# Optimization experiments

Hardware: AMD Instinct MI355X
Metric: run time of the kernel (lower is better)

Reference implementation:

```python
import jax, jax.numpy as jnp
import numpy as np

EMB = 1024
H = 16
DH = 64


def setup_inputs() -> dict:
    key = jax.random.key(0)
    ks = jax.random.split(key, 9)
    s = 1.0 / np.sqrt(EMB)
    so = 1.0 / np.sqrt(H * DH)
    return {
        "x": jax.random.normal(ks[0], (4, 2048, EMB), dtype=jnp.float32),
        "Wq": jax.random.uniform(ks[1], (H * DH, EMB), jnp.float32, -s, s),
        "bq": jax.random.uniform(ks[2], (H * DH,), jnp.float32, -s, s),
        "Wk": jax.random.uniform(ks[3], (H * DH, EMB), jnp.float32, -s, s),
        "bk": jax.random.uniform(ks[4], (H * DH,), jnp.float32, -s, s),
        "Wv": jax.random.uniform(ks[5], (H * DH, EMB), jnp.float32, -s, s),
        "bv": jax.random.uniform(ks[6], (H * DH,), jnp.float32, -s, s),
        "Wo": jax.random.uniform(ks[7], (EMB, H * DH), jnp.float32, -so, so),
        "bo": jax.random.uniform(ks[8], (EMB,), jnp.float32, -so, so),
    }


def reference(x, Wq, bq, Wk, bk, Wv, bv, Wo, bo):
    B, S, E = x.shape
    # project and split heads: [B, H, S, Dh]
    def proj(W, b):
        return (jnp.einsum('bse,de->bsd', x, W) + b).reshape(B, S, H, DH).transpose(0, 2, 1, 3)
    q = proj(Wq, bq)
    k = proj(Wk, bk)
    v = proj(Wv, bv)
    scores = jnp.einsum('bhsd,bhtd->bhst', q / jnp.sqrt(jnp.float32(DH)), k)
    attn = jax.nn.softmax(scores, axis=-1)
    out = jnp.einsum('bhst,bhtd->bhsd', attn, v)  # [B,H,S,Dh]
    out = out.transpose(0, 2, 1, 3).reshape(B, S, H * DH)
    return jnp.einsum('bsd,ed->bse', out, Wo) + bo
```

## Files before the change

kernel.cpp:

```cpp
#include <hip/hip_runtime.h>
#include <hip/hip_bf16.h>
#include <stdint.h>

typedef __bf16 bf16x8 __attribute__((ext_vector_type(8)));
typedef float f32x4 __attribute__((ext_vector_type(4)));
typedef float f32x16 __attribute__((ext_vector_type(16)));
typedef uint32_t u32x4 __attribute__((ext_vector_type(4)));

__device__ __forceinline__ ushort f2bf(float f) {
  uint32_t u = __builtin_bit_cast(uint32_t, f);
  u += 0x7FFFu + ((u >> 16) & 1u);
  return (ushort)(u >> 16);
}

__device__ __forceinline__ uint32_t cvtpk(float lo, float hi) {
  uint32_t r;
  asm("v_cvt_pk_bf16_f32 %0, %1, %2" : "=v"(r) : "v"(lo), "v"(hi));
  return r;
}

__device__ __forceinline__ void p32swap(uint32_t& x, uint32_t& y) {
  asm("v_permlane32_swap_b32 %0, %1" : "+v"(x), "+v"(y));
}

__device__ __forceinline__ void gload16(const void* g, void* l) {
  auto gp = reinterpret_cast<const __attribute__((address_space(1))) char*>(
      reinterpret_cast<uintptr_t>(g));
  auto lp = reinterpret_cast<__attribute__((address_space(3))) char*>(
      reinterpret_cast<uintptr_t>(l));
  __builtin_amdgcn_global_load_lds(gp, lp, 16, 0, 0);
}

__device__ __forceinline__ f32x4 mfma16(bf16x8 a, bf16x8 b, f32x4 c) {
  return __builtin_amdgcn_mfma_f32_16x16x32_bf16(a, b, c, 0, 0, 0);
}
__device__ __forceinline__ f32x16 mfma32(bf16x8 a, bf16x8 b, f32x16 c) {
  return __builtin_amdgcn_mfma_f32_32x32x16_bf16(a, b, c, 0, 0, 0);
}

#define VMW(n) do { asm volatile("s_waitcnt vmcnt(" #n ")" ::: "memory"); \
                    __builtin_amdgcn_sched_barrier(0); } while (0)
#define SBAR __builtin_amdgcn_s_barrier()
#define SCHED0 __builtin_amdgcn_sched_barrier(0)

__global__ void cast_all(const float* __restrict__ x,  const float* __restrict__ wq,
                         const float* __restrict__ wk, const float* __restrict__ wv,
                         const float* __restrict__ wo,
                         ushort* __restrict__ xb, ushort* __restrict__ wqkv,
                         ushort* __restrict__ wob) {
  int bid = blockIdx.x;
  const float* src; ushort* dst; int base;
  if (bid < 8192)       { src = x;  dst = xb;              base = bid; }
  else if (bid < 9216)  { src = wq; dst = wqkv;            base = bid - 8192; }
  else if (bid < 10240) { src = wk; dst = wqkv + 1048576;  base = bid - 9216; }
  else if (bid < 11264) { src = wv; dst = wqkv + 2097152;  base = bid - 10240; }
  else                  { src = wo; dst = wob;             base = bid - 11264; }
  int i = (base * 256 + threadIdx.x) * 4;
  float4 v = *(const float4*)(src + i);
  ushort4 o;
  o.x = f2bf(v.x); o.y = f2bf(v.y); o.z = f2bf(v.z); o.w = f2bf(v.w);
  *(ushort4*)(dst + i) = o;
}

template <int MODE>
__global__ __launch_bounds__(512, 2) void gemm_k(
    const ushort* __restrict__ A, const ushort* __restrict__ Bm,
    const float* __restrict__ b0, const float* __restrict__ b1,
    ushort* __restrict__ qo, ushort* __restrict__ ko, ushort* __restrict__ vo,
    float* __restrict__ fo)
{
  __shared__ ushort As[3][128 * 64];
  __shared__ ushort Bs[3][256 * 64];
  const int tid = threadIdx.x;
  const int lane = tid & 63, wid = tid >> 6;
  const int wr = wid >> 2, wc = wid & 3;
  const int l15 = lane & 15, l4 = lane >> 4;

  const int wg = blockIdx.x, nwg = gridDim.x, qch = nwg >> 3;
  const int lid = (wg & 7) * qch + (wg >> 3);
  const int bx = (MODE == 2) ? (lid >> 4) : (lid >> 6);
  const int by = (MODE == 2) ? (lid & 15) : (lid & 63);
  const int m0 = by * 128, n0 = bx * 256;

  const char* Ag = (const char*)(A + (size_t)m0 * 1024);
  const char* Wg = (const char*)(Bm + (size_t)n0 * 1024);

  f32x4 acc[4][4] = {};

  const int soff = tid * 16;

  auto STAGE = [&](int d, int kt) {
    const int k0b = kt * 128;
#pragma unroll
    for (int s = 0; s < 2; ++s) {
      int off = soff + s * 8192;
      int row = off >> 7, cb = off & 127;
      int sc = cb ^ ((row & 7) << 4);
      gload16(Ag + (size_t)row * 2048 + k0b + sc, (char*)As[d] + off);
    }
#pragma unroll
    for (int s = 0; s < 4; ++s) {
      int off = soff + s * 8192;
      int row = off >> 7, cb = off & 127;
      int sc = cb ^ ((row & 7) << 4);
      gload16(Wg + (size_t)row * 2048 + k0b + sc, (char*)Bs[d] + off);
    }
  };

  bf16x8 af[4][2], bfr[4][2];

  auto EXTRACT = [&](int d) {
#pragma unroll
    for (int mt = 0; mt < 4; ++mt) {
      int row = wr * 64 + mt * 16 + l15;
      int sw = (row & 7) << 4;
#pragma unroll
      for (int kk = 0; kk < 2; ++kk)
        af[mt][kk] = *(const bf16x8*)((const char*)As[d] + row * 128 +
                                      ((kk * 64 + l4 * 16) ^ sw));
    }
#pragma unroll
    for (int nt = 0; nt < 4; ++nt) {
      int row = wc * 64 + nt * 16 + l15;
      int sw = (row & 7) << 4;
#pragma unroll
      for (int kk = 0; kk < 2; ++kk)
        bfr[nt][kk] = *(const bf16x8*)((const char*)Bs[d] + row * 128 +
                                       ((kk * 64 + l4 * 16) ^ sw));
    }
  };

  auto MFMAS = [&]() {
    __builtin_amdgcn_s_setprio(1);
#pragma unroll
    for (int kk = 0; kk < 2; ++kk)
#pragma unroll
      for (int mt = 0; mt < 4; ++mt)
#pragma unroll
        for (int nt = 0; nt < 4; ++nt)
          acc[mt][nt] = mfma16(af[mt][kk], bfr[nt][kk], acc[mt][nt]);
    __builtin_amdgcn_s_setprio(0);
  };

  STAGE(0, 0);
  STAGE(1, 1);
  VMW(6); SBAR; SCHED0;

#pragma unroll
  for (int t = 0; t < 14; ++t) {
    STAGE((t + 2) % 3, t + 2);
    EXTRACT(t % 3);
    MFMAS();
    VMW(6);
    SBAR; SCHED0;
  }
  EXTRACT(2); MFMAS(); VMW(0); SBAR; SCHED0;
  EXTRACT(0); MFMAS();

  if (MODE == 2) {
    const int seg = m0 >> 10;
    ushort* dst = seg ? ko : qo;
    const float* bptr = seg ? b1 : b0;
    const float sc = seg ? 1.0f : 0.18033688011112042f;
#pragma unroll
    for (int mt = 0; mt < 4; ++mt) {
      int mrow = m0 + wr * 64 + mt * 16 + l4 * 4;
      int nl = mrow & 1023;
      int h = nl >> 6, d0 = nl & 63;
      float4 bias = *(const float4*)(bptr + nl);
#pragma unroll
      for (int nt = 0; nt < 4; ++nt) {
        int s = n0 + wc * 64 + nt * 16 + l15;
        int b = s >> 11, sl = s & 2047;
        ushort4 pk;
        pk.x = f2bf((acc[mt][nt][0] + bias.x) * sc);
        pk.y = f2bf((acc[mt][nt][1] + bias.y) * sc);
        pk.z = f2bf((acc[mt][nt][2] + bias.z) * sc);
        pk.w = f2bf((acc[mt][nt][3] + bias.w) * sc);
        *(ushort4*)(dst + (size_t)((b * 16 + h) * 2048 + sl) * 64 + d0) = pk;
      }
    }
  } else if (MODE == 0) {
#pragma unroll
    for (int nt = 0; nt < 4; ++nt) {
      int nl = n0 + wc * 64 + nt * 16 + l15;
      int h = nl >> 6, dd = nl & 63;
      float bias = b0[nl];
#pragma unroll
      for (int mt = 0; mt < 4; ++mt) {
        int m = m0 + wr * 64 + mt * 16 + l4 * 4;
        int b = m >> 11, s = m & 2047;
        ushort4 pk;
        pk.x = f2bf(acc[mt][nt][0] + bias);
        pk.y = f2bf(acc[mt][nt][1] + bias);
        pk.z = f2bf(acc[mt][nt][2] + bias);
        pk.w = f2bf(acc[mt][nt][3] + bias);
        *(ushort4*)(vo + (size_t)((b * 16 + h) * 64 + dd) * 2048 + s) = pk;
      }
    }
  } else {
#pragma unroll
    for (int nt = 0; nt < 4; ++nt) {
      int n = n0 + wc * 64 + nt * 16 + l15;
      float bias = b0[n];
#pragma unroll
      for (int mt = 0; mt < 4; ++mt) {
        int m = m0 + wr * 64 + mt * 16 + l4 * 4;
#pragma unroll
        for (int r = 0; r < 4; ++r)
          fo[(size_t)(m + r) * 1024 + n] = acc[mt][nt][r] + bias;
      }
    }
  }
}

__global__ __launch_bounds__(256, 2) void attn_k(
    const ushort* __restrict__ Q, const ushort* __restrict__ K,
    const ushort* __restrict__ V, ushort* __restrict__ O)
{
  __shared__ ushort KVs[2][8192];
  const int tid = threadIdx.x, lane = tid & 63;
  const int l31 = lane & 31, hi = lane >> 5;
  const int w = tid >> 6;
  const int bh = blockIdx.x;
  const int b = bh >> 4, h = bh & 15;
  const int q0 = blockIdx.y * 256 + w * 64;
  const ushort* Qh = Q + (size_t)bh * 131072;
  const ushort* Kh = K + (size_t)bh * 131072;
  const ushort* Vh = V + (size_t)bh * 131072;

  bf16x8 qf[2][4];
#pragma unroll
  for (int g = 0; g < 2; ++g)
#pragma unroll
    for (int c = 0; c < 4; ++c)
      qf[g][c] = *(const bf16x8*)(Qh + (size_t)(q0 + g * 32 + l31) * 64 + c * 16 + hi * 8);

  u32x4 onebits;
  onebits[0] = 0x3F803F80u; onebits[1] = 0x3F803F80u;
  onebits[2] = 0x3F803F80u; onebits[3] = 0x3F803F80u;
  const bf16x8 ones = __builtin_bit_cast(bf16x8, onebits);

  f32x16 oacc[2][2] = {};
  float lrun[2] = {0.f, 0.f};

  const int sw = (l31 & 7) << 4;
  const int loff = tid * 16;
  const int srow = loff >> 7, scolb = loff & 127;

  auto STAGE = [&](int buf, int j) {
    char* base = (char*)KVs[buf];
#pragma unroll
    for (int sh = 0; sh < 2; ++sh) {
      int row = srow + sh * 32;
      int off = loff + sh * 4096;
      int sc = scolb ^ ((row & 7) << 4);
      gload16((const char*)Kh + (size_t)j * 8192 + row * 128 + sc, base + off);
      gload16((const char*)Vh + (size_t)row * 4096 + j * 128 + sc, base + 8192 + off);
    }
  };

  STAGE(0, 0);
  __syncthreads();
  int cur = 0;

  for (int j = 0; j < 32; ++j) {
    if (j < 31) STAGE(cur ^ 1, j + 1);
    const char* Kb = (const char*)KVs[cur];
    const char* Vb = Kb + 8192;

    f32x16 sacc[2][2] = {};
    __builtin_amdgcn_s_setprio(1);
#pragma unroll
    for (int t = 0; t < 2; ++t)
#pragma unroll
      for (int c = 0; c < 4; ++c) {
        bf16x8 kfr = *(const bf16x8*)(Kb + (t * 32 + l31) * 128 +
                                      ((c * 32 + hi * 16) ^ sw));
        sacc[0][t] = mfma32(kfr, qf[0][c], sacc[0][t]);
        sacc[1][t] = mfma32(kfr, qf[1][c], sacc[1][t]);
      }
    __builtin_amdgcn_s_setprio(0);

    bf16x8 pb[2][4];
#pragma unroll
    for (int g = 0; g < 2; ++g) {
#pragma unroll
      for (int t = 0; t < 2; ++t)
#pragma unroll
        for (int r = 0; r < 16; ++r)
          sacc[g][t][r] = __builtin_amdgcn_exp2f(sacc[g][t][r]);

      uint32_t wlo[2][4], whi[2][4];
#pragma unroll
      for (int t = 0; t < 2; ++t)
#pragma unroll
        for (int gg = 0; gg < 4; ++gg) {
          wlo[t][gg] = cvtpk(sacc[g][t][gg * 4 + 0], sacc[g][t][gg * 4 + 1]);
          whi[t][gg] = cvtpk(sacc[g][t][gg * 4 + 2], sacc[g][t][gg * 4 + 3]);
        }
#pragma unroll
      for (int c = 0; c < 4; ++c) {
        const int t = c >> 1, gb = (c & 1) * 2;
        uint32_t x0 = wlo[t][gb], y0 = wlo[t][gb + 1];
        p32swap(x0, y0);
        uint32_t x1 = whi[t][gb], y1 = whi[t][gb + 1];
        p32swap(x1, y1);
        u32x4 wv_;
        wv_[0] = x0; wv_[1] = x1; wv_[2] = y0; wv_[3] = y1;
        pb[g][c] = __builtin_bit_cast(bf16x8, wv_);
      }
    }

    f32x16 ssacc[2] = {};
    __builtin_amdgcn_s_setprio(1);
#pragma unroll
    for (int dt = 0; dt < 2; ++dt)
#pragma unroll
      for (int c = 0; c < 4; ++c) {
        bf16x8 vfr = *(const bf16x8*)(Vb + (dt * 32 + l31) * 128 +
                                      ((c * 32 + hi * 16) ^ sw));
        oacc[0][dt] = mfma32(vfr, pb[0][c], oacc[0][dt]);
        oacc[1][dt] = mfma32(vfr, pb[1][c], oacc[1][dt]);
      }
#pragma unroll
    for (int c = 0; c < 4; ++c) {
      ssacc[0] = mfma32(ones, pb[0][c], ssacc[0]);
      ssacc[1] = mfma32(ones, pb[1][c], ssacc[1]);
    }
    __builtin_amdgcn_s_setprio(0);
    lrun[0] += ssacc[0][0];
    lrun[1] += ssacc[1][0];

    __syncthreads();
    cur ^= 1;
  }

#pragma unroll
  for (int g = 0; g < 2; ++g) {
    float linv = 1.0f / lrun[g];
    ushort* Ob = O + (size_t)(b * 2048 + q0 + g * 32 + l31) * 1024 + h * 64;
#pragma unroll
    for (int dt = 0; dt < 2; ++dt)
#pragma unroll
      for (int gg = 0; gg < 4; ++gg) {
        ushort4 o4;
        o4.x = f2bf(oacc[g][dt][gg * 4 + 0] * linv);
        o4.y = f2bf(oacc[g][dt][gg * 4 + 1] * linv);
        o4.z = f2bf(oacc[g][dt][gg * 4 + 2] * linv);
        o4.w = f2bf(oacc[g][dt][gg * 4 + 3] * linv);
        *(ushort4*)(Ob + dt * 32 + gg * 8 + hi * 4) = o4;
      }
  }
}

extern "C" void kernel_launch(void* const* d_in, const int* in_sizes, int n_in,
                              void* d_out, int out_size, void* d_ws, size_t ws_size,
                              hipStream_t stream)
{
  const float* x  = (const float*)d_in[0];
  const float* Wq = (const float*)d_in[1];
  const float* bq = (const float*)d_in[2];
  const float* Wk = (const float*)d_in[3];
  const float* bk = (const float*)d_in[4];
  const float* Wv = (const float*)d_in[5];
  const float* bv = (const float*)d_in[6];
  const float* Wo = (const float*)d_in[7];
  const float* bo = (const float*)d_in[8];
  float* out = (float*)d_out;
  ushort* ws = (ushort*)d_ws;

  ushort* xb   = ws;
  ushort* wqkv = ws + 8388608;
  ushort* wo   = ws + 11534336;
  ushort* qb   = ws + 12582912;
  ushort* kb   = ws + 20971520;
  ushort* vb   = ws + 29360128;

  cast_all<<<12288, 256, 0, stream>>>(x, Wq, Wk, Wv, Wo, xb, wqkv, wo);

  gemm_k<2><<<512, 512, 0, stream>>>(wqkv, xb, bq, bk, qb, kb, nullptr, nullptr);
  gemm_k<0><<<256, 512, 0, stream>>>(xb, wqkv + 2097152, bv, nullptr,
                                     nullptr, nullptr, vb, nullptr);
  attn_k<<<dim3(64, 8), 256, 0, stream>>>(qb, kb, vb, xb);
  gemm_k<1><<<256, 512, 0, stream>>>(xb, wo, bo, nullptr, nullptr, nullptr, nullptr, out);
}
```

Measured before the change: 167.8 us.

## Merge QK and V projection GEMMs into one launch with split-phase K-loop

Combines the two projection GEMM launches (Q/K and V) into a single 768-workgroup kernel that branches on block index, removing one launch and the tail between them. The GEMM main loop is also reorganized into two half-phases: each stages and extracts half of the B tile and issues half the MFMAs, with extra barriers and lgkmcnt waits in between. The intent is to interleave global loads, LDS reads and MFMAs more finely, at the cost of twice as many barriers per k-step.

```diff
diff --git a/kernel.cpp b/kernel.cpp
--- a/kernel.cpp
+++ b/kernel.cpp
@@ -38,6 +38,8 @@
   return __builtin_amdgcn_mfma_f32_32x32x16_bf16(a, b, c, 0, 0, 0);
 }
 
+#define LGKM0 do { asm volatile("s_waitcnt lgkmcnt(0)" ::: "memory"); \
+                   __builtin_amdgcn_sched_barrier(0); } while (0)
 #define VMW(n) do { asm volatile("s_waitcnt vmcnt(" #n ")" ::: "memory"); \
                     __builtin_amdgcn_sched_barrier(0); } while (0)
 #define SBAR __builtin_amdgcn_s_barrier()
@@ -62,12 +64,105 @@
   *(ushort4*)(dst + i) = o;
 }
 
-template <int MODE>
-__global__ __launch_bounds__(512, 2) void gemm_k(
-    const ushort* __restrict__ A, const ushort* __restrict__ Bm,
-    const float* __restrict__ b0, const float* __restrict__ b1,
-    ushort* __restrict__ qo, ushort* __restrict__ ko, ushort* __restrict__ vo,
-    float* __restrict__ fo)
+#define GEMM_PHASED_BODY                                                       \
+  f32x4 acc[4][4] = {};                                                        \
+  const int soff = tid * 16;                                                   \
+  auto STAGE_A = [&](int d, int kt) {                                          \
+    const int k0b = kt * 128;                                                  \
+    _Pragma("unroll")                                                          \
+    for (int s = 0; s < 2; ++s) {                                              \
+      int off = soff + s * 8192;                                               \
+      int row = off >> 7, cb = off & 127;                                      \
+      int sc = cb ^ ((row & 7) << 4);                                          \
+      gload16(Ag + (size_t)row * 2048 + k0b + sc, (char*)As[d] + off);         \
+    }                                                                          \
+    { int off = soff;                                                          \
+      int row = off >> 7, cb = off & 127;                                      \
+      int sc = cb ^ ((row & 7) << 4);                                          \
+      gload16(Wg + (size_t)row * 2048 + k0b + sc, (char*)Bs[d] + off); }       \
+  };                                                                           \
+  auto STAGE_B = [&](int d, int kt) {                                          \
+    const int k0b = kt * 128;                                                  \
+    _Pragma("unroll")                                                          \
+    for (int s = 1; s < 4; ++s) {                                              \
+      int off = soff + s * 8192;                                               \
+      int row = off >> 7, cb = off & 127;                                      \
+      int sc = cb ^ ((row & 7) << 4);                                          \
+      gload16(Wg + (size_t)row * 2048 + k0b + sc, (char*)Bs[d] + off);         \
+    }                                                                          \
+  };                                                                           \
+  bf16x8 af[4][2], bfr[4][2];                                                  \
+  auto EXTRACT_A = [&](int d) {                                                \
+    _Pragma("unroll")                                                          \
+    for (int mt = 0; mt < 4; ++mt) {                                           \
+      int row = wr * 64 + mt * 16 + l15;                                       \
+      int sw = (row & 7) << 4;                                                 \
+      _Pragma("unroll")                                                        \
+      for (int kk = 0; kk < 2; ++kk)                                           \
+        af[mt][kk] = *(const bf16x8*)((const char*)As[d] + row * 128 +         \
+                                      ((kk * 64 + l4 * 16) ^ sw));             \
+    }                                                                          \
+    _Pragma("unroll")                                                          \
+    for (int nt = 0; nt < 2; ++nt) {                                           \
+      int row = wc * 64 + nt * 16 + l15;                                       \
+      int sw = (row & 7) << 4;                                                 \
+      _Pragma("unroll")                                                        \
+      for (int kk = 0; kk < 2; ++kk)                                           \
+        bfr[nt][kk] = *(const bf16x8*)((const char*)Bs[d] + row * 128 +        \
+                                       ((kk * 64 + l4 * 16) ^ sw));            \
+    }                                                                          \
+  };                                                                           \
+  auto EXTRACT_B = [&](int d) {                                                \
+    _Pragma("unroll")                                                          \
+    for (int nt = 2; nt < 4; ++nt) {                                           \
+      int row = wc * 64 + nt * 16 + l15;                                       \
+      int sw = (row & 7) << 4;                                                 \
+      _Pragma("unroll")                                                        \
+      for (int kk = 0; kk < 2; ++kk)                                           \
+        bfr[nt][kk] = *(const bf16x8*)((const char*)Bs[d] + row * 128 +        \
+                                       ((kk * 64 + l4 * 16) ^ sw));            \
+    }                                                                          \
+  };                                                                           \
+  auto MFMA_H = [&](int nlo) {                                                 \
+    __builtin_amdgcn_s_setprio(1);                                             \
+    _Pragma("unroll")                                                          \
+    for (int kk = 0; kk < 2; ++kk)                                             \
+      _Pragma("unroll")                                                        \
+      for (int mt = 0; mt < 4; ++mt)                                           \
+        _Pragma("unroll")                                                      \
+        for (int nt2 = 0; nt2 < 2; ++nt2)                                      \
+          acc[mt][nlo + nt2] =                                                 \
+              mfma16(af[mt][kk], bfr[nlo + nt2][kk], acc[mt][nlo + nt2]);      \
+    __builtin_amdgcn_s_setprio(0);                                             \
+  };                                                                           \
+  STAGE_A(0, 0); STAGE_B(0, 0);                                                \
+  STAGE_A(1, 1); STAGE_B(1, 1);                                                \
+  VMW(6); SBAR; SCHED0;                                                        \
+  _Pragma("unroll")                                                            \
+  for (int t = 0; t < 14; ++t) {                                               \
+    const int d = t % 3, dn = (t + 2) % 3;                                     \
+    STAGE_A(dn, t + 2);                                                        \
+    EXTRACT_A(d);                                                              \
+    SBAR; LGKM0;                                                               \
+    MFMA_H(0);                                                                 \
+    SBAR;                                                                      \
+    STAGE_B(dn, t + 2);                                                        \
+    EXTRACT_B(d);                                                              \
+    SBAR; LGKM0;                                                               \
+    MFMA_H(2);                                                                 \
+    VMW(6);                                                                    \
+    SBAR;                                                                      \
+  }                                                                            \
+  EXTRACT_A(2); SBAR; LGKM0; MFMA_H(0); SBAR;                                  \
+  EXTRACT_B(2); SBAR; LGKM0; MFMA_H(2); VMW(0); SBAR;                          \
+  EXTRACT_A(0); LGKM0; MFMA_H(0);                                              \
+  EXTRACT_B(0); LGKM0; MFMA_H(2);
+
+__global__ __launch_bounds__(512, 2) void gemm_qkv(
+    const ushort* __restrict__ xb, const ushort* __restrict__ wqkv,
+    const float* __restrict__ bq, const float* __restrict__ bk,
+    const float* __restrict__ bv,
+    ushort* __restrict__ qo, ushort* __restrict__ ko, ushort* __restrict__ vo)
 {
   __shared__ ushort As[3][128 * 64];
   __shared__ ushort Bs[3][256 * 64];
@@ -76,91 +171,29 @@
   const int wr = wid >> 2, wc = wid & 3;
   const int l15 = lane & 15, l4 = lane >> 4;
 
-  const int wg = blockIdx.x, nwg = gridDim.x, qch = nwg >> 3;
-  const int lid = (wg & 7) * qch + (wg >> 3);
-  const int bx = (MODE == 2) ? (lid >> 4) : (lid >> 6);
-  const int by = (MODE == 2) ? (lid & 15) : (lid & 63);
-  const int m0 = by * 128, n0 = bx * 256;
-
-  const char* Ag = (const char*)(A + (size_t)m0 * 1024);
-  const char* Wg = (const char*)(Bm + (size_t)n0 * 1024);
-
-  f32x4 acc[4][4] = {};
-
-  const int soff = tid * 16;
-
-  auto STAGE = [&](int d, int kt) {
-    const int k0b = kt * 128;
-#pragma unroll
-    for (int s = 0; s < 2; ++s) {
-      int off = soff + s * 8192;
-      int row = off >> 7, cb = off & 127;
-      int sc = cb ^ ((row & 7) << 4);
-      gload16(Ag + (size_t)row * 2048 + k0b + sc, (char*)As[d] + off);
-    }
-#pragma unroll
-    for (int s = 0; s < 4; ++s) {
-      int off = soff + s * 8192;
-      int row = off >> 7, cb = off & 127;
-      int sc = cb ^ ((row & 7) << 4);
-      gload16(Wg + (size_t)row * 2048 + k0b + sc, (char*)Bs[d] + off);
-    }
-  };
-
-  bf16x8 af[4][2], bfr[4][2];
-
-  auto EXTRACT = [&](int d) {
-#pragma unroll
-    for (int mt = 0; mt < 4; ++mt) {
-      int row = wr * 64 + mt * 16 + l15;
-      int sw = (row & 7) << 4;
-#pragma unroll
-      for (int kk = 0; kk < 2; ++kk)
-        af[mt][kk] = *(const bf16x8*)((const char*)As[d] + row * 128 +
-                                      ((kk * 64 + l4 * 16) ^ sw));
-    }
-#pragma unroll
-    for (int nt = 0; nt < 4; ++nt) {
-      int row = wc * 64 + nt * 16 + l15;
-      int sw = (row & 7) << 4;
-#pragma unroll
-      for (int kk = 0; kk < 2; ++kk)
-        bfr[nt][kk] = *(const bf16x8*)((const char*)Bs[d] + row * 128 +
-                                       ((kk * 64 + l4 * 16) ^ sw));
-    }
-  };
-
-  auto MFMAS = [&]() {
-    __builtin_amdgcn_s_setprio(1);
-#pragma unroll
-    for (int kk = 0; kk < 2; ++kk)
-#pragma unroll
-      for (int mt = 0; mt < 4; ++mt)
-#pragma unroll
-        for (int nt = 0; nt < 4; ++nt)
-          acc[mt][nt] = mfma16(af[mt][kk], bfr[nt][kk], acc[mt][nt]);
-    __builtin_amdgcn_s_setprio(0);
-  };
-
-  STAGE(0, 0);
-  STAGE(1, 1);
-  VMW(6); SBAR; SCHED0;
-
-#pragma unroll
-  for (int t = 0; t < 14; ++t) {
-    STAGE((t + 2) % 3, t + 2);
-    EXTRACT(t % 3);
-    MFMAS();
-    VMW(6);
-    SBAR; SCHED0;
+  const int wg = blockIdx.x;
+  const bool isQK = wg < 512;
+  int m0, n0;
+  const char *Ag, *Wg;
+  if (isQK) {
+    const int lid = (wg & 7) * 64 + (wg >> 3);
+    m0 = (lid & 15) * 128; n0 = (lid >> 4) * 256;
+    Ag = (const char*)(wqkv + (size_t)m0 * 1024);
+    Wg = (const char*)(xb + (size_t)n0 * 1024);
+  } else {
+    const int sg = wg - 512;
+    const int lid = (sg & 7) * 32 + (sg >> 3);
+    m0 = (lid & 63) * 128; n0 = (lid >> 6) * 256;
+    Ag = (const char*)(xb + (size_t)m0 * 1024);
+    Wg = (const char*)(wqkv + 2097152 + (size_t)n0 * 1024);
   }
-  EXTRACT(2); MFMAS(); VMW(0); SBAR; SCHED0;
-  EXTRACT(0); MFMAS();
-
-  if (MODE == 2) {
+
+  GEMM_PHASED_BODY
+
+  if (isQK) {
     const int seg = m0 >> 10;
     ushort* dst = seg ? ko : qo;
-    const float* bptr = seg ? b1 : b0;
+    const float* bptr = seg ? bk : bq;
     const float sc = seg ? 1.0f : 0.18033688011112042f;
 #pragma unroll
     for (int mt = 0; mt < 4; ++mt) {
@@ -180,12 +213,12 @@
         *(ushort4*)(dst + (size_t)((b * 16 + h) * 2048 + sl) * 64 + d0) = pk;
       }
     }
-  } else if (MODE == 0) {
+  } else {
 #pragma unroll
     for (int nt = 0; nt < 4; ++nt) {
       int nl = n0 + wc * 64 + nt * 16 + l15;
       int h = nl >> 6, dd = nl & 63;
-      float bias = b0[nl];
+      float bias = bv[nl];
 #pragma unroll
       for (int mt = 0; mt < 4; ++mt) {
         int m = m0 + wr * 64 + mt * 16 + l4 * 4;
@@ -198,18 +231,40 @@
         *(ushort4*)(vo + (size_t)((b * 16 + h) * 64 + dd) * 2048 + s) = pk;
       }
     }
-  } else {
-#pragma unroll
-    for (int nt = 0; nt < 4; ++nt) {
-      int n = n0 + wc * 64 + nt * 16 + l15;
-      float bias = b0[n];
-#pragma unroll
-      for (int mt = 0; mt < 4; ++mt) {
-        int m = m0 + wr * 64 + mt * 16 + l4 * 4;
-#pragma unroll
-        for (int r = 0; r < 4; ++r)
-          fo[(size_t)(m + r) * 1024 + n] = acc[mt][nt][r] + bias;
-      }
+  }
+}
+
+__global__ __launch_bounds__(512, 2) void gemm_out(
+    const ushort* __restrict__ A, const ushort* __restrict__ Bm,
+    const float* __restrict__ b0, float* __restrict__ fo)
+{
+  __shared__ ushort As[3][128 * 64];
+  __shared__ ushort Bs[3][256 * 64];
+  const int tid = threadIdx.x;
+  const int lane = tid & 63, wid = tid >> 6;
+  const int wr = wid >> 2, wc = wid & 3;
+  const int l15 = lane & 15, l4 = lane >> 4;
+
+  const int wg = blockIdx.x;
+  const int lid = (wg & 7) * 32 + (wg >> 3);
+  const int bx = lid >> 6, by = lid & 63;
+  const int m0 = by * 128, n0 = bx * 256;
+
+  const char* Ag = (const char*)(A + (size_t)m0 * 1024);
+  const char* Wg = (const char*)(Bm + (size_t)n0 * 1024);
+
+  GEMM_PHASED_BODY
+
+#pragma unroll
+  for (int nt = 0; nt < 4; ++nt) {
+    int n = n0 + wc * 64 + nt * 16 + l15;
+    float bias = b0[n];
+#pragma unroll
+    for (int mt = 0; mt < 4; ++mt) {
+      int m = m0 + wr * 64 + mt * 16 + l4 * 4;
+#pragma unroll
+      for (int r = 0; r < 4; ++r)
+        fo[(size_t)(m + r) * 1024 + n] = acc[mt][nt][r] + bias;
     }
   }
 }
@@ -379,9 +434,7 @@
 
   cast_all<<<12288, 256, 0, stream>>>(x, Wq, Wk, Wv, Wo, xb, wqkv, wo);
 
-  gemm_k<2><<<512, 512, 0, stream>>>(wqkv, xb, bq, bk, qb, kb, nullptr, nullptr);
-  gemm_k<0><<<256, 512, 0, stream>>>(xb, wqkv + 2097152, bv, nullptr,
-                                     nullptr, nullptr, vb, nullptr);
+  gemm_qkv<<<768, 512, 0, stream>>>(xb, wqkv, bq, bk, bv, qb, kb, vb);
   attn_k<<<dim3(64, 8), 256, 0, stream>>>(qb, kb, vb, xb);
-  gemm_k<1><<<256, 512, 0, stream>>>(xb, wo, bo, nullptr, nullptr, nullptr, nullptr, out);
-}
+  gemm_out<<<256, 512, 0, stream>>>(xb, wo, bo, out);
+}
```

New measurement: 169.5 us. Within noise of the previous version (+1.0%).
